# Kernel optimization log

Hardware: AMD Instinct MI355X
Metric: run time of the kernel (lower is better)

Reference implementation:

```python
import jax, jax.numpy as jnp
import numpy as np
from jax import lax

DN = ('NCHW', 'OIHW', 'NCHW')
T_STEPS = 10      # len(predict_timesteps), unit-spaced
SUBSTEPS = 2      # RK4 substeps per unit time interval


def _conv(x, w, b, pad):
    y = lax.conv_general_dilated(x, w, (1, 1), ((pad, pad), (pad, pad)), dimension_numbers=DN)
    return y + b[None, :, None, None]


def _deconv(x, w, b):
    # stride-2 transposed conv (k=4, p=1 equivalent): input dilation 2, pad 2
    y = lax.conv_general_dilated(x, w, (1, 1), ((2, 2), (2, 2)), lhs_dilation=(2, 2), dimension_numbers=DN)
    return y + b[None, :, None, None]


def setup_inputs() -> dict:
    key = jax.random.key(0)
    ks = jax.random.split(key, 16)
    f32 = jnp.float32
    d = {}
    d['h_s0'] = jax.random.normal(ks[0], (4, 64, 32, 32), dtype=f32)
    # ODE dynamics convs: 64 -> 64, 3x3
    for i in range(4):
        d[f'w{i+1}'] = jax.random.normal(ks[1 + i], (64, 64, 3, 3), dtype=f32) * 0.05
        d[f'b{i+1}'] = jnp.zeros((64,), dtype=f32)
    # decoding stages
    d['s1_w'] = jax.random.normal(ks[8], (32, 64, 4, 4), dtype=f32) * 0.1
    d['s1_b'] = jnp.zeros((32,), dtype=f32)
    d['s2_w'] = jax.random.normal(ks[9], (16, 32, 4, 4), dtype=f32) * 0.1
    d['s2_b'] = jnp.zeros((16,), dtype=f32)
    d['s3_w'] = jax.random.normal(ks[10], (1, 16, 3, 3), dtype=f32) * 0.1
    d['s3_b'] = jnp.zeros((1,), dtype=f32)
    return d


def reference(h_s0, w1, b1, w2, b2, w3, b3, w4, b4, s1_w, s1_b, s2_w, s2_b, s3_w, s3_b):
    def f(y):  # Decoder_ODEModel.forward (autonomous: t unused)
        y = jnp.tanh(_conv(y, w1, b1, 1))
        y = jnp.tanh(_conv(y, w2, b2, 1))
        y = jnp.tanh(_conv(y, w3, b3, 1))
        return _conv(y, w4, b4, 1)

    dt = jnp.float32(1.0 / SUBSTEPS)

    def rk4(y):
        k1 = f(y)
        k2 = f(y + 0.5 * dt * k1)
        k3 = f(y + 0.5 * dt * k2)
        k4 = f(y + dt * k3)
        return y + (dt / 6.0) * (k1 + 2.0 * k2 + 2.0 * k3 + k4)

    def interval(y, _):
        for _ in range(SUBSTEPS):
            y = rk4(y)
        return y, y

    _, ys = lax.scan(interval, h_s0, None, length=T_STEPS - 1)
    outs = jnp.concatenate([h_s0[None], ys], axis=0)  # [T, B, C, H, W]

    T, B, C, H, W = outs.shape
    x = outs.reshape(T * B, C, H, W)
    x = jax.nn.leaky_relu(_deconv(x, s1_w, s1_b), 0.2)   # 32x32 -> 64x64
    x = jax.nn.leaky_relu(_deconv(x, s2_w, s2_b), 0.2)   # 64x64 -> 128x128
    x = _conv(x, s3_w, s3_b, 1)                           # -> 1 channel
    return x.reshape(T, B, x.shape[1], x.shape[2], x.shape[3])
```

## Files before the change

### kernel.cpp

```cpp
#include <hip/hip_runtime.h>
#include <hip/hip_bf16.h>
#include <stdint.h>

typedef __attribute__((ext_vector_type(8))) short short8;
typedef __attribute__((ext_vector_type(4))) float f32x4;
typedef __attribute__((ext_vector_type(4))) int int4v;

__device__ __forceinline__ float bf2f(unsigned short u) {
  union { unsigned int i; float f; } v; v.i = ((unsigned int)u) << 16; return v.f;
}
__device__ __forceinline__ unsigned short f2bf(float f) {
  union { float f; unsigned int i; } v; v.f = f;
  unsigned int i = v.i;
  i += 0x7FFFu + ((i >> 16) & 1u);
  return (unsigned short)(i >> 16);
}
__device__ __forceinline__ float tanh_fast(float x) {
  float e = __expf(2.0f * x);
  return 1.0f - 2.0f / (e + 1.0f);
}
__device__ __forceinline__ uint32_t pack_pair(float v) {
  unsigned short hi = f2bf(v);
  unsigned short lo = f2bf(v - bf2f(hi));
  return (uint32_t)hi | ((uint32_t)lo << 16);
}

__global__ void prep_weights(const float* __restrict__ w1, const float* __restrict__ w2,
                             const float* __restrict__ w3, const float* __restrict__ w4,
                             const float* __restrict__ s1w, const float* __restrict__ s2w,
                             const float* __restrict__ s3w,
                             unsigned short* __restrict__ wimg,
                             float* __restrict__ s1wt, float* __restrict__ s2wt,
                             float* __restrict__ s3wt) {
  int t = blockIdx.x * 256 + threadIdx.x;
  if (t < 147456) {
    int l = t / 36864;
    int oc = (t / 576) & 63;
    int ic = (t / 9) & 63;
    int tap = t % 9;
    const float* w = (l == 0) ? w1 : (l == 1) ? w2 : (l == 2) ? w3 : w4;
    float v = w[(oc * 64 + ic) * 9 + tap];
    unsigned short hi = f2bf(v);
    unsigned short lo = f2bf(v - bf2f(hi));
    int icb = ic >> 5, icm = ic & 31;
    int idx = (icb * 64 + oc) * 288 + tap * 32 + icm;
    wimg[l * 73728 + idx]         = hi;
    wimg[l * 73728 + 36864 + idx] = lo;
  } else if (t < 180224) {
    int u = t - 147456;
    int oc = u & 31, ic = (u >> 5) & 63, kk = u >> 11;
    int ky = kk >> 2, kx = kk & 3;
    s1wt[(kk * 64 + ic) * 32 + oc] = s1w[((oc * 64 + ic) * 4 + ky) * 4 + kx];
  } else if (t < 188416) {
    int u = t - 180224;
    int oc = u & 15, ic = (u >> 4) & 31, kk = u >> 9;
    int ky = kk >> 2, kx = kk & 3;
    s2wt[(kk * 32 + ic) * 16 + oc] = s2w[((oc * 32 + ic) * 4 + ky) * 4 + kx];
  } else if (t < 188560) {
    int u = t - 188416;
    int ic = u & 15, kk = u >> 4;
    int ky = kk / 3, kx = kk % 3;
    s3wt[u] = s3w[ic * 9 + ky * 3 + kx];
  }
}

__global__ void prep_state(const float* __restrict__ src,
                           uint32_t* __restrict__ s0, float* __restrict__ outs0) {
  int t = blockIdx.x * 256 + threadIdx.x;
  int c = t & 63, w = (t >> 6) & 31, h = (t >> 11) & 31, b = t >> 16;
  float v = src[((b * 64 + c) * 32 + h) * 32 + w];
  s0[t] = pack_pair(v);
  outs0[t] = v;
}

#define A_BUF 34816
#define A_ARR 17408
#define WBASE 69632
#define W_ARR 40960
#define CONV_LDS 151552

__device__ __forceinline__ void conv_body(
    uint8_t* lds, int b, int h0, int cur, int full,
    const uint32_t* __restrict__ inP,
    const unsigned short* __restrict__ wimg, const float* __restrict__ bias,
    uint32_t* __restrict__ outP,
    float* Y, float* R, float* __restrict__ outsPtr, int mode) {
  const int tid = threadIdx.x;
  uint8_t* A = lds + cur * A_BUF;
  uint8_t* An = lds + (cur ^ 1) * A_BUF;

  const int nitems = full ? 1088 : 544;
  for (int idx = tid; idx < nitems; idx += 1024) {
    int c = idx & 7;
    int w1 = (idx >> 3) % 34;
    int rsel = (idx >> 3) / 34;
    int row = full ? rsel : rsel * 3;
    int hp = h0 - 1 + row;
    int w = w1 - 1;
    short8 hi8 = {0, 0, 0, 0, 0, 0, 0, 0};
    short8 lo8 = {0, 0, 0, 0, 0, 0, 0, 0};
    if (hp >= 0 && hp < 32 && w >= 0 && w < 32) {
      const uint64_t* sp = (const uint64_t*)(inP + (((b * 32 + hp) * 32 + w) * 64 + c * 8));
#pragma unroll
      for (int q = 0; q < 4; ++q) {
        uint64_t pk2 = __hip_atomic_load(sp + q, __ATOMIC_RELAXED,
                                         __HIP_MEMORY_SCOPE_AGENT);
        uint32_t p0 = (uint32_t)pk2, p1 = (uint32_t)(pk2 >> 32);
        hi8[q * 2]     = (short)(p0 & 0xFFFFu);
        lo8[q * 2]     = (short)(p0 >> 16);
        hi8[q * 2 + 1] = (short)(p1 & 0xFFFFu);
        lo8[q * 2 + 1] = (short)(p1 >> 16);
      }
    }
    const int pix = row * 34 + w1;
    const int off = pix * 128 + ((c ^ (pix & 7)) * 16);
    *(short8*)(A + off) = hi8;
    *(short8*)(A + A_ARR + off) = lo8;
  }
  int4v wpre[5];
#pragma unroll
  for (int k = 0; k < 5; ++k) {
    int idx = tid + k * 1024;
    if (idx < 4608) {
      int arr = idx / 2304;
      int r2 = idx - arr * 2304;
      int oc = r2 / 36;
      int ch = r2 - oc * 36;
      int4v v0 = *(const int4v*)(wimg + (((arr * 2 + 0) * 64 + oc) * 288 + ch * 8));
      *(int4v*)(lds + WBASE + arr * W_ARR + oc * 640 + ((ch ^ (oc & 7)) * 16)) = v0;
      wpre[k] = *(const int4v*)(wimg + (((arr * 2 + 1) * 64 + oc) * 288 + ch * 8));
    }
  }
  __syncthreads();

  const int lane = tid & 63;
  const int wv = tid >> 6;
  const int mq = wv & 3;
  const int ng = wv >> 2;
  const int lmod = lane & 15;
  const int lg = lane >> 4;
  const int P = mq * 16 + lmod;
  const int r = P >> 5;
  const int c0 = P & 31;
  const int oc = ng * 16 + lmod;

  f32x4 acc = (f32x4){0.f, 0.f, 0.f, 0.f};

#pragma unroll
  for (int icb = 0; icb < 2; ++icb) {
    if (icb == 1) {
      __syncthreads();
#pragma unroll
      for (int k = 0; k < 5; ++k) {
        int idx = tid + k * 1024;
        if (idx < 4608) {
          int arr = idx / 2304;
          int r2 = idx - arr * 2304;
          int oco = r2 / 36;
          int ch = r2 - oco * 36;
          *(int4v*)(lds + WBASE + arr * W_ARR + oco * 640 + ((ch ^ (oco & 7)) * 16)) = wpre[k];
        }
      }
      __syncthreads();
    }
#pragma unroll
    for (int tap = 0; tap < 9; ++tap) {
      const int dy = tap / 3, dx = tap % 3;
      const int pix = (r + dy) * 34 + (c0 + dx);
      const int chunk = icb * 4 + lg;
      const int abyte = pix * 128 + ((chunk ^ (pix & 7)) * 16);
      short8 ah = *(const short8*)(A + abyte);
      short8 al = *(const short8*)(A + A_ARR + abyte);
      const int slot = tap * 4 + lg;
      const int wb = WBASE + oc * 640 + ((slot ^ (oc & 7)) * 16);
      short8 bh = *(const short8*)(lds + wb);
      short8 bl = *(const short8*)(lds + wb + W_ARR);
      acc = __builtin_amdgcn_mfma_f32_16x16x32_bf16(ah, bh, acc, 0, 0, 0);
      acc = __builtin_amdgcn_mfma_f32_16x16x32_bf16(al, bh, acc, 0, 0, 0);
      acc = __builtin_amdgcn_mfma_f32_16x16x32_bf16(ah, bl, acc, 0, 0, 0);
    }
  }

  const float bz = bias[oc];
#pragma unroll
  for (int j = 0; j < 4; ++j) {
    const int px = mq * 16 + lg * 4 + j;
    const int e = (b * 1024 + h0 * 32 + px) * 64 + oc;
    float kv = acc[j] + bz;
    float z;
    if (mode == 0) {
      z = tanh_fast(kv);
    } else if (mode == 1) {
      z = fmaf(0.25f, kv, Y[j]);
      R[j] = fmaf(1.0f / 12.0f, kv, Y[j]);
    } else if (mode == 2 || mode == 3) {
      float cz = (mode == 2) ? 0.25f : 0.5f;
      z = fmaf(cz, kv, Y[j]);
      R[j] = fmaf(1.0f / 6.0f, kv, R[j]);
    } else {
      z = fmaf(1.0f / 12.0f, kv, R[j]);
      Y[j] = z;
      if (outsPtr) outsPtr[e] = z;
    }
    uint32_t pk = pack_pair(z);
    __hip_atomic_store(&outP[e], pk, __ATOMIC_RELAXED, __HIP_MEMORY_SCOPE_AGENT);
    const int pix = (1 + (px >> 5)) * 34 + (px & 31) + 1;
    const int off = pix * 128 + (((oc >> 3) ^ (pix & 7)) * 16) + (oc & 7) * 2;
    *(unsigned short*)(An + off)         = (unsigned short)(pk & 0xFFFFu);
    *(unsigned short*)(An + A_ARR + off) = (unsigned short)(pk >> 16);
  }
}

__global__ __launch_bounds__(1024) void ode_persist(
    const unsigned short* __restrict__ wimg,
    const float* __restrict__ b1, const float* __restrict__ b2,
    const float* __restrict__ b3, const float* __restrict__ b4,
    uint32_t* __restrict__ S0, uint32_t* __restrict__ S1,
    uint32_t* __restrict__ T0, uint32_t* __restrict__ T1,
    float* __restrict__ outs, int* progress) {
  extern __shared__ uint8_t lds[];
  const int blk = blockIdx.x;
  const int b = blk >> 4;
  const int rp = blk & 15;
  const int h0 = rp << 1;
  const int nbA = (rp > 0) ? blk - 1 : -1;
  const int nbB = (rp < 15) ? blk + 1 : -1;

  const unsigned short* Wl[4] = {wimg, wimg + 73728, wimg + 147456, wimg + 221184};
  const float* Bl[4] = {b1, b2, b3, b4};

  if (threadIdx.x < 128) {
    int t = threadIdx.x;
    int chunk = t & 7;
    int col = ((t >> 3) & 1) * 33;
    int row = 1 + ((t >> 4) & 1);
    int arr = (t >> 5) & 1;
    int buf = (t >> 6) & 1;
    int pix = row * 34 + col;
    *(int4v*)(lds + buf * A_BUF + arr * A_ARR + pix * 128 +
              ((chunk ^ (pix & 7)) * 16)) = (int4v){0, 0, 0, 0};
  }
  __syncthreads();

  const int lane = threadIdx.x & 63;
  const int wv = threadIdx.x >> 6;
  const int mq = wv & 3, ng = wv >> 2;
  const int lmod = lane & 15, lg = lane >> 4;
  float Y[4], R[4];
#pragma unroll
  for (int j = 0; j < 4; ++j) {
    const int e = (b * 1024 + h0 * 32 + mq * 16 + lg * 4 + j) * 64 + ng * 16 + lmod;
    Y[j] = outs[e];
    R[j] = 0.f;
  }

  int done = 0;
  int cur = 0;
  for (int step = 1; step <= 18; ++step) {
    for (int sub = 0; sub < 4; ++sub) {
      for (int layer = 0; layer < 4; ++layer) {
        const uint32_t* inP;
        uint32_t* outP;
        int mode;
        float* op = nullptr;
        if (layer == 0) {
          inP = (sub == 0) ? S0 : S1; outP = T0; mode = 0;
        } else if (layer == 1) {
          inP = T0; outP = T1; mode = 0;
        } else if (layer == 2) {
          inP = T1; outP = T0; mode = 0;
        } else {
          inP = T0; outP = (sub == 3) ? S0 : S1; mode = 1 + sub;
          if (sub == 3 && (step & 1) == 0) op = outs + (size_t)(step >> 1) * 262144;
        }
        if (threadIdx.x == 0 && done > 0) {
          if (nbA >= 0)
            while (__hip_atomic_load(&progress[nbA], __ATOMIC_RELAXED,
                                     __HIP_MEMORY_SCOPE_AGENT) < done)
              __builtin_amdgcn_s_sleep(2);
          if (nbB >= 0)
            while (__hip_atomic_load(&progress[nbB], __ATOMIC_RELAXED,
                                     __HIP_MEMORY_SCOPE_AGENT) < done)
              __builtin_amdgcn_s_sleep(2);
        }
        __builtin_amdgcn_sched_barrier(0);
        __syncthreads();

        conv_body(lds, b, h0, cur, done == 0, inP, Wl[layer], Bl[layer], outP,
                  Y, R, op, mode);

        __syncthreads();
        ++done;
        cur ^= 1;
        if (threadIdx.x == 0) {
          __hip_atomic_store(&progress[blk], done, __ATOMIC_RELEASE,
                             __HIP_MEMORY_SCOPE_AGENT);
        }
      }
    }
  }
}

__global__ __launch_bounds__(256) void dec_s1(const float* __restrict__ in,
                                              const float* __restrict__ wt,
                                              const float* __restrict__ bs,
                                              float* __restrict__ out) {
  __shared__ float wl[4][64][32];
  const int tid = threadIdx.x;
  const int bl = blockIdx.x & 127;
  const int par = (blockIdx.x >> 7) & 3;
  const int n = blockIdx.x >> 9;
  const int py = par >> 1, px = par & 1;
#pragma unroll
  for (int k = 0; k < 32; ++k) {
    int s = tid + k * 256;
    int oc_ = s & 31, ic = (s >> 5) & 63, tp = s >> 11;
    int kk = (py + 2 * (tp >> 1)) * 4 + (px + 2 * (tp & 1));
    wl[tp][ic][oc_] = wt[(kk * 64 + ic) * 32 + oc_];
  }
  __syncthreads();
  const int oc = tid & 31;
  const int pos = bl * 8 + (tid >> 5);
  const int my = pos >> 5, mx = pos & 31;
  float a = bs[oc];
#pragma unroll
  for (int ay = 0; ay < 2; ++ay) {
    int iy = my + py - 1 + ay;
    if ((unsigned)iy >= 32u) continue;
#pragma unroll
    for (int ax = 0; ax < 2; ++ax) {
      int ix = mx + px - 1 + ax;
      if ((unsigned)ix >= 32u) continue;
      const float4* xp = (const float4*)(in + ((n * 32 + iy) * 32 + ix) * 64);
      const int tp = ay * 2 + ax;
#pragma unroll
      for (int i4 = 0; i4 < 16; ++i4) {
        float4 xv = xp[i4];
        a = fmaf(xv.x, wl[tp][i4 * 4 + 0][oc], a);
        a = fmaf(xv.y, wl[tp][i4 * 4 + 1][oc], a);
        a = fmaf(xv.z, wl[tp][i4 * 4 + 2][oc], a);
        a = fmaf(xv.w, wl[tp][i4 * 4 + 3][oc], a);
      }
    }
  }
  const int oy = 2 * my + py, ox = 2 * mx + px;
  out[((n * 64 + oy) * 64 + ox) * 32 + oc] = (a > 0.f) ? a : 0.2f * a;
}

__global__ __launch_bounds__(256) void dec_s2(const float* __restrict__ in,
                                              const float* __restrict__ wt,
                                              const float* __restrict__ bs,
                                              float* __restrict__ out) {
  __shared__ float wl[4][32][16];
  const int tid = threadIdx.x;
  const int bl = blockIdx.x & 255;
  const int par = (blockIdx.x >> 8) & 3;
  const int n = blockIdx.x >> 10;
  const int py = par >> 1, px = par & 1;
#pragma unroll
  for (int k = 0; k < 8; ++k) {
    int s = tid + k * 256;
    int oc_ = s & 15, ic = (s >> 4) & 31, tp = s >> 9;
    int kk = (py + 2 * (tp >> 1)) * 4 + (px + 2 * (tp & 1));
    wl[tp][ic][oc_] = wt[(kk * 32 + ic) * 16 + oc_];
  }
  __syncthreads();
  const int oc = tid & 15;
  const int pos = bl * 16 + (tid >> 4);
  const int my = pos >> 6, mx = pos & 63;
  float a = bs[oc];
#pragma unroll
  for (int ay = 0; ay < 2; ++ay) {
    int iy = my + py - 1 + ay;
    if ((unsigned)iy >= 64u) continue;
#pragma unroll
    for (int ax = 0; ax < 2; ++ax) {
      int ix = mx + px - 1 + ax;
      if ((unsigned)ix >= 64u) continue;
      const float4* xp = (const float4*)(in + ((n * 64 + iy) * 64 + ix) * 32);
      const int tp = ay * 2 + ax;
#pragma unroll
      for (int i4 = 0; i4 < 8; ++i4) {
        float4 xv = xp[i4];
        a = fmaf(xv.x, wl[tp][i4 * 4 + 0][oc], a);
        a = fmaf(xv.y, wl[tp][i4 * 4 + 1][oc], a);
        a = fmaf(xv.z, wl[tp][i4 * 4 + 2][oc], a);
        a = fmaf(xv.w, wl[tp][i4 * 4 + 3][oc], a);
      }
    }
  }
  const int oy = 2 * my + py, ox = 2 * mx + px;
  out[((n * 128 + oy) * 128 + ox) * 16 + oc] = (a > 0.f) ? a : 0.2f * a;
}

__global__ __launch_bounds__(256) void dec_s3(const float* __restrict__ in,
                                              const float* __restrict__ wt,
                                              const float* __restrict__ bs,
                                              float* __restrict__ out) {
  int t = blockIdx.x * 256 + threadIdx.x;
  int ox = t & 127, oy = (t >> 7) & 127, n = t >> 14;
  float a = bs[0];
#pragma unroll
  for (int ky = 0; ky < 3; ++ky) {
    int iy = oy + ky - 1;
    if ((unsigned)iy >= 128u) continue;
#pragma unroll
    for (int kx = 0; kx < 3; ++kx) {
      int ix = ox + kx - 1;
      if ((unsigned)ix >= 128u) continue;
      const float4* xp = (const float4*)(in + ((n * 128 + iy) * 128 + ix) * 16);
      const float4* wp = (const float4*)(wt + (ky * 3 + kx) * 16);
#pragma unroll
      for (int i4 = 0; i4 < 4; ++i4) {
        float4 xv = xp[i4], wv = wp[i4];
        a = fmaf(xv.x, wv.x, a);
        a = fmaf(xv.y, wv.y, a);
        a = fmaf(xv.z, wv.z, a);
        a = fmaf(xv.w, wv.w, a);
      }
    }
  }
  out[n * 16384 + oy * 128 + ox] = a;
}

extern "C" void kernel_launch(void* const* d_in, const int* in_sizes, int n_in,
                              void* d_out, int out_size, void* d_ws, size_t ws_size,
                              hipStream_t stream) {
  (void)in_sizes; (void)n_in; (void)out_size; (void)ws_size;
  (void)hipFuncSetAttribute((const void*)ode_persist,
                            hipFuncAttributeMaxDynamicSharedMemorySize, CONV_LDS);

  uint8_t* ws = (uint8_t*)d_ws;
  uint32_t* S0 = (uint32_t*)(ws + 0);
  uint32_t* S1 = (uint32_t*)(ws + 1048576);
  uint32_t* T0 = (uint32_t*)(ws + 2097152);
  uint32_t* T1 = (uint32_t*)(ws + 3145728);
  unsigned short* WIMG = (unsigned short*)(ws + 4194304);
  float* s1wt = (float*)(ws + 4784128);
  float* s2wt = (float*)(ws + 4915200);
  float* s3wt = (float*)(ws + 4947968);
  int* progress = (int*)(ws + 4980736);
  float* outs = (float*)(ws + 5242880);
  float* d1 = (float*)(ws + 16777216);
  float* d2 = (float*)(ws + 18874368);

  const float* h_s0 = (const float*)d_in[0];
  const float* wode[4] = {(const float*)d_in[1], (const float*)d_in[3],
                          (const float*)d_in[5], (const float*)d_in[7]};
  const float* bode[4] = {(const float*)d_in[2], (const float*)d_in[4],
                          (const float*)d_in[6], (const float*)d_in[8]};
  const float* s1w = (const float*)d_in[9];
  const float* s1b = (const float*)d_in[10];
  const float* s2w = (const float*)d_in[11];
  const float* s2b = (const float*)d_in[12];
  const float* s3w = (const float*)d_in[13];
  const float* s3b = (const float*)d_in[14];

  (void)hipMemsetAsync(progress, 0, 64 * sizeof(int), stream);
  prep_weights<<<737, 256, 0, stream>>>(wode[0], wode[1], wode[2], wode[3],
                                        s1w, s2w, s3w, WIMG, s1wt, s2wt, s3wt);
  prep_state<<<1024, 256, 0, stream>>>(h_s0, S0, outs);

  ode_persist<<<dim3(64), dim3(1024), CONV_LDS, stream>>>(
      WIMG, bode[0], bode[1], bode[2], bode[3],
      S0, S1, T0, T1, outs, progress);

  for (int t0 = 0; t0 < 10; ++t0) {
    dec_s1<<<2048, 256, 0, stream>>>(outs + (size_t)t0 * 262144, s1wt, s1b, d1);
    dec_s2<<<4096, 256, 0, stream>>>(d1, s2wt, s2b, d2);
    dec_s3<<<256, 256, 0, stream>>>(d2, s3wt, s3b,
                                    (float*)d_out + (size_t)t0 * 65536);
  }
}
```

Measured before the change: 2.675 ms.

## Split conv K dimension across waves with 2x2 register tiles and LDS reduction

Weights are no longer staged through LDS. Each wave now reads its B fragments directly from global memory and computes a 2x2 block of 16x16 tiles. The 18 tap/channel slices are split among four wave groups, and the partial sums are reduced through an LDS scratch area, where wave group 0 runs the epilogue. This removes the per-layer weight staging, two barriers and the weight LDS footprint, and it reuses A and B fragments across tiles. The cost is an extra reduction pass and barrier, direct global weight loads that depend on cache hits, only a quarter of the waves doing the epilogue, and a launch-bounds hint that raises register pressure.

```diff
diff --git a/kernel.cpp b/kernel.cpp
--- a/kernel.cpp
+++ b/kernel.cpp
@@ -75,16 +75,50 @@
 
 #define A_BUF 34816
 #define A_ARR 17408
-#define WBASE 69632
-#define W_ARR 40960
-#define CONV_LDS 151552
+#define REDB 69632
+#define CONV_LDS 118784
+
+__device__ __forceinline__ void slice_run(
+    const uint8_t* A, const unsigned short* __restrict__ wimgL, int s,
+    int mt, int lmod, int lg, int wo00, int wo01, int wo10, int wo11,
+    f32x4& a00, f32x4& a01, f32x4& a10, f32x4& a11) {
+  const int icb = (s >= 9) ? 1 : 0;
+  const int tp = s - icb * 9;
+  const int dy = tp / 3, dx = tp % 3;
+  const int d = icb * 18432 + tp * 32;
+  short8 bh0 = *(const short8*)(wimgL + wo00 + d);
+  short8 bh1 = *(const short8*)(wimgL + wo01 + d);
+  short8 bl0 = *(const short8*)(wimgL + wo10 + d);
+  short8 bl1 = *(const short8*)(wimgL + wo11 + d);
+  const int chunk = icb * 4 + lg;
+  const int pix0 = (mt + dy) * 34 + (lmod + dx);
+  const int pix1 = pix0 + 16;
+  const int ab0 = pix0 * 128 + ((chunk ^ (pix0 & 7)) * 16);
+  const int ab1 = pix1 * 128 + ((chunk ^ (pix1 & 7)) * 16);
+  short8 ah0 = *(const short8*)(A + ab0);
+  short8 al0 = *(const short8*)(A + A_ARR + ab0);
+  short8 ah1 = *(const short8*)(A + ab1);
+  short8 al1 = *(const short8*)(A + A_ARR + ab1);
+  a00 = __builtin_amdgcn_mfma_f32_16x16x32_bf16(ah0, bh0, a00, 0, 0, 0);
+  a00 = __builtin_amdgcn_mfma_f32_16x16x32_bf16(al0, bh0, a00, 0, 0, 0);
+  a00 = __builtin_amdgcn_mfma_f32_16x16x32_bf16(ah0, bl0, a00, 0, 0, 0);
+  a01 = __builtin_amdgcn_mfma_f32_16x16x32_bf16(ah0, bh1, a01, 0, 0, 0);
+  a01 = __builtin_amdgcn_mfma_f32_16x16x32_bf16(al0, bh1, a01, 0, 0, 0);
+  a01 = __builtin_amdgcn_mfma_f32_16x16x32_bf16(ah0, bl1, a01, 0, 0, 0);
+  a10 = __builtin_amdgcn_mfma_f32_16x16x32_bf16(ah1, bh0, a10, 0, 0, 0);
+  a10 = __builtin_amdgcn_mfma_f32_16x16x32_bf16(al1, bh0, a10, 0, 0, 0);
+  a10 = __builtin_amdgcn_mfma_f32_16x16x32_bf16(ah1, bl0, a10, 0, 0, 0);
+  a11 = __builtin_amdgcn_mfma_f32_16x16x32_bf16(ah1, bh1, a11, 0, 0, 0);
+  a11 = __builtin_amdgcn_mfma_f32_16x16x32_bf16(al1, bh1, a11, 0, 0, 0);
+  a11 = __builtin_amdgcn_mfma_f32_16x16x32_bf16(ah1, bl1, a11, 0, 0, 0);
+}
 
 __device__ __forceinline__ void conv_body(
     uint8_t* lds, int b, int h0, int cur, int full,
     const uint32_t* __restrict__ inP,
-    const unsigned short* __restrict__ wimg, const float* __restrict__ bias,
+    const unsigned short* __restrict__ wimgL, const float* __restrict__ bias,
     uint32_t* __restrict__ outP,
-    float* Y, float* R, float* __restrict__ outsPtr, int mode) {
+    f32x4* Y, f32x4* R, float* __restrict__ outsPtr, int mode) {
   const int tid = threadIdx.x;
   uint8_t* A = lds + cur * A_BUF;
   uint8_t* An = lds + (cur ^ 1) * A_BUF;
@@ -117,101 +151,99 @@
     *(short8*)(A + off) = hi8;
     *(short8*)(A + A_ARR + off) = lo8;
   }
-  int4v wpre[5];
-#pragma unroll
-  for (int k = 0; k < 5; ++k) {
-    int idx = tid + k * 1024;
-    if (idx < 4608) {
-      int arr = idx / 2304;
-      int r2 = idx - arr * 2304;
-      int oc = r2 / 36;
-      int ch = r2 - oc * 36;
-      int4v v0 = *(const int4v*)(wimg + (((arr * 2 + 0) * 64 + oc) * 288 + ch * 8));
-      *(int4v*)(lds + WBASE + arr * W_ARR + oc * 640 + ((ch ^ (oc & 7)) * 16)) = v0;
-      wpre[k] = *(const int4v*)(wimg + (((arr * 2 + 1) * 64 + oc) * 288 + ch * 8));
-    }
-  }
   __syncthreads();
 
   const int lane = tid & 63;
   const int wv = tid >> 6;
-  const int mq = wv & 3;
-  const int ng = wv >> 2;
+  const int kq = wv >> 2;
+  const int tl = wv & 3;
+  const int mt = tl >> 1;
+  const int nt = tl & 1;
   const int lmod = lane & 15;
   const int lg = lane >> 4;
-  const int P = mq * 16 + lmod;
-  const int r = P >> 5;
-  const int c0 = P & 31;
-  const int oc = ng * 16 + lmod;
-
-  f32x4 acc = (f32x4){0.f, 0.f, 0.f, 0.f};
-
-#pragma unroll
-  for (int icb = 0; icb < 2; ++icb) {
-    if (icb == 1) {
-      __syncthreads();
-#pragma unroll
-      for (int k = 0; k < 5; ++k) {
-        int idx = tid + k * 1024;
-        if (idx < 4608) {
-          int arr = idx / 2304;
-          int r2 = idx - arr * 2304;
-          int oco = r2 / 36;
-          int ch = r2 - oco * 36;
-          *(int4v*)(lds + WBASE + arr * W_ARR + oco * 640 + ((ch ^ (oco & 7)) * 16)) = wpre[k];
+
+  const int wo00 = (nt * 32 + lmod) * 288 + lg * 8;
+  const int wo01 = wo00 + 16 * 288;
+  const int wo10 = wo00 + 36864;
+  const int wo11 = wo10 + 16 * 288;
+
+  f32x4 a00 = {0.f,0.f,0.f,0.f}, a01 = {0.f,0.f,0.f,0.f};
+  f32x4 a10 = {0.f,0.f,0.f,0.f}, a11 = {0.f,0.f,0.f,0.f};
+
+  if (kq < 2) {
+    const int s0 = kq * 5;
+#pragma unroll
+    for (int u = 0; u < 5; ++u)
+      slice_run(A, wimgL, s0 + u, mt, lmod, lg, wo00, wo01, wo10, wo11,
+                a00, a01, a10, a11);
+  } else {
+    const int s0 = 10 + (kq - 2) * 4;
+#pragma unroll
+    for (int u = 0; u < 4; ++u)
+      slice_run(A, wimgL, s0 + u, mt, lmod, lg, wo00, wo01, wo10, wo11,
+                a00, a01, a10, a11);
+  }
+
+  if (kq > 0) {
+    uint8_t* rb = lds + REDB + ((kq - 1) * 4 + tl) * 4096 + lane * 16;
+    *(f32x4*)(rb)        = a00;
+    *(f32x4*)(rb + 1024) = a01;
+    *(f32x4*)(rb + 2048) = a10;
+    *(f32x4*)(rb + 3072) = a11;
+  }
+  __syncthreads();
+
+  if (kq == 0) {
+#pragma unroll
+    for (int p = 0; p < 3; ++p) {
+      const uint8_t* rb = lds + REDB + (p * 4 + tl) * 4096 + lane * 16;
+      a00 += *(const f32x4*)(rb);
+      a01 += *(const f32x4*)(rb + 1024);
+      a10 += *(const f32x4*)(rb + 2048);
+      a11 += *(const f32x4*)(rb + 3072);
+    }
+#pragma unroll
+    for (int msub = 0; msub < 2; ++msub) {
+#pragma unroll
+      for (int nsub = 0; nsub < 2; ++nsub) {
+        const int q = msub * 2 + nsub;
+        f32x4 accv = (q == 0) ? a00 : (q == 1) ? a01 : (q == 2) ? a10 : a11;
+        const int oc = nt * 32 + nsub * 16 + lmod;
+        const float bz = bias[oc];
+#pragma unroll
+        for (int j = 0; j < 4; ++j) {
+          const int px = mt * 32 + msub * 16 + lg * 4 + j;
+          const int e = (b * 1024 + h0 * 32 + px) * 64 + oc;
+          float kv = accv[j] + bz;
+          float z;
+          if (mode == 0) {
+            z = tanh_fast(kv);
+          } else if (mode == 1) {
+            z = fmaf(0.25f, kv, Y[q][j]);
+            R[q][j] = fmaf(1.0f / 12.0f, kv, Y[q][j]);
+          } else if (mode == 2 || mode == 3) {
+            float cz = (mode == 2) ? 0.25f : 0.5f;
+            z = fmaf(cz, kv, Y[q][j]);
+            R[q][j] = fmaf(1.0f / 6.0f, kv, R[q][j]);
+          } else {
+            z = fmaf(1.0f / 12.0f, kv, R[q][j]);
+            Y[q][j] = z;
+            if (outsPtr) outsPtr[e] = z;
+          }
+          uint32_t pk = pack_pair(z);
+          __hip_atomic_store(&outP[e], pk, __ATOMIC_RELAXED,
+                             __HIP_MEMORY_SCOPE_AGENT);
+          const int pix = (1 + (px >> 5)) * 34 + (px & 31) + 1;
+          const int off = pix * 128 + (((oc >> 3) ^ (pix & 7)) * 16) + (oc & 7) * 2;
+          *(unsigned short*)(An + off)         = (unsigned short)(pk & 0xFFFFu);
+          *(unsigned short*)(An + A_ARR + off) = (unsigned short)(pk >> 16);
         }
       }
-      __syncthreads();
-    }
-#pragma unroll
-    for (int tap = 0; tap < 9; ++tap) {
-      const int dy = tap / 3, dx = tap % 3;
-      const int pix = (r + dy) * 34 + (c0 + dx);
-      const int chunk = icb * 4 + lg;
-      const int abyte = pix * 128 + ((chunk ^ (pix & 7)) * 16);
-      short8 ah = *(const short8*)(A + abyte);
-      short8 al = *(const short8*)(A + A_ARR + abyte);
-      const int slot = tap * 4 + lg;
-      const int wb = WBASE + oc * 640 + ((slot ^ (oc & 7)) * 16);
-      short8 bh = *(const short8*)(lds + wb);
-      short8 bl = *(const short8*)(lds + wb + W_ARR);
-      acc = __builtin_amdgcn_mfma_f32_16x16x32_bf16(ah, bh, acc, 0, 0, 0);
-      acc = __builtin_amdgcn_mfma_f32_16x16x32_bf16(al, bh, acc, 0, 0, 0);
-      acc = __builtin_amdgcn_mfma_f32_16x16x32_bf16(ah, bl, acc, 0, 0, 0);
-    }
-  }
-
-  const float bz = bias[oc];
-#pragma unroll
-  for (int j = 0; j < 4; ++j) {
-    const int px = mq * 16 + lg * 4 + j;
-    const int e = (b * 1024 + h0 * 32 + px) * 64 + oc;
-    float kv = acc[j] + bz;
-    float z;
-    if (mode == 0) {
-      z = tanh_fast(kv);
-    } else if (mode == 1) {
-      z = fmaf(0.25f, kv, Y[j]);
-      R[j] = fmaf(1.0f / 12.0f, kv, Y[j]);
-    } else if (mode == 2 || mode == 3) {
-      float cz = (mode == 2) ? 0.25f : 0.5f;
-      z = fmaf(cz, kv, Y[j]);
-      R[j] = fmaf(1.0f / 6.0f, kv, R[j]);
-    } else {
-      z = fmaf(1.0f / 12.0f, kv, R[j]);
-      Y[j] = z;
-      if (outsPtr) outsPtr[e] = z;
-    }
-    uint32_t pk = pack_pair(z);
-    __hip_atomic_store(&outP[e], pk, __ATOMIC_RELAXED, __HIP_MEMORY_SCOPE_AGENT);
-    const int pix = (1 + (px >> 5)) * 34 + (px & 31) + 1;
-    const int off = pix * 128 + (((oc >> 3) ^ (pix & 7)) * 16) + (oc & 7) * 2;
-    *(unsigned short*)(An + off)         = (unsigned short)(pk & 0xFFFFu);
-    *(unsigned short*)(An + A_ARR + off) = (unsigned short)(pk >> 16);
-  }
-}
-
-__global__ __launch_bounds__(1024) void ode_persist(
+    }
+  }
+}
+
+__global__ __launch_bounds__(1024, 4) void ode_persist(
     const unsigned short* __restrict__ wimg,
     const float* __restrict__ b1, const float* __restrict__ b2,
     const float* __restrict__ b3, const float* __restrict__ b4,
@@ -244,14 +276,25 @@
 
   const int lane = threadIdx.x & 63;
   const int wv = threadIdx.x >> 6;
-  const int mq = wv & 3, ng = wv >> 2;
+  const int kq = wv >> 2, tl = wv & 3;
+  const int mt = tl >> 1, nt = tl & 1;
   const int lmod = lane & 15, lg = lane >> 4;
-  float Y[4], R[4];
-#pragma unroll
-  for (int j = 0; j < 4; ++j) {
-    const int e = (b * 1024 + h0 * 32 + mq * 16 + lg * 4 + j) * 64 + ng * 16 + lmod;
-    Y[j] = outs[e];
-    R[j] = 0.f;
+  f32x4 Y[4], R[4];
+#pragma unroll
+  for (int q = 0; q < 4; ++q) { Y[q] = (f32x4){0,0,0,0}; R[q] = (f32x4){0,0,0,0}; }
+  if (kq == 0) {
+#pragma unroll
+    for (int msub = 0; msub < 2; ++msub)
+#pragma unroll
+      for (int nsub = 0; nsub < 2; ++nsub) {
+        const int q = msub * 2 + nsub;
+#pragma unroll
+        for (int j = 0; j < 4; ++j) {
+          const int px = mt * 32 + msub * 16 + lg * 4 + j;
+          const int e = (b * 1024 + h0 * 32 + px) * 64 + nt * 32 + nsub * 16 + lmod;
+          Y[q][j] = outs[e];
+        }
+      }
   }
 
   int done = 0;
```

After: 6.850 ms. +156.1%, slower.
